# Kernel optimization log

Hardware: AMD Instinct MI355X
Metric: run time of the kernel (lower is better)

The kernel has to match this reference:

```python
import jax, jax.numpy as jnp
import numpy as np

B, N, M = 2, 4096, 4096
QUERY_DIM, CONTEXT_DIM = 512, 768
H, D = 8, 64
INNER = H * D


def setup_inputs() -> dict:
    key = jax.random.key(0)
    ks = jax.random.split(key, 8)
    x = jax.random.normal(ks[0], (B, N, QUERY_DIM), dtype=jnp.float32)
    context_tensor = jax.random.normal(ks[1], (B, M, CONTEXT_DIM), dtype=jnp.float32)
    mask = jax.random.randint(ks[2], (B, M), 0, 2) > 0  # bool [B, M]
    s = 0.02
    Wq = jax.random.normal(ks[3], (QUERY_DIM, INNER), dtype=jnp.float32) * s
    Wk = jax.random.normal(ks[4], (CONTEXT_DIM, INNER), dtype=jnp.float32) * s
    Wv = jax.random.normal(ks[5], (CONTEXT_DIM, INNER), dtype=jnp.float32) * s
    Wo = jax.random.normal(ks[6], (INNER, QUERY_DIM), dtype=jnp.float32) * s
    bo = jnp.zeros((QUERY_DIM,), dtype=jnp.float32)
    return {"x": x, "context_tensor": context_tensor, "mask": mask,
            "Wq": Wq, "Wk": Wk, "Wv": Wv, "Wo": Wo, "bo": bo}


def reference(x, context_tensor, mask, Wq, Wk, Wv, Wo, bo):
    scale = D ** (-0.5)
    # projections -> [B, T, H, D]
    q = (x @ Wq).reshape(B, N, H, D)
    k = (context_tensor @ Wk).reshape(B, M, H, D)
    v = (context_tensor @ Wv).reshape(B, M, H, D)
    # scores [B, H, N, M]
    attn = jnp.einsum('bnhd,bmhd->bhnm', q, k) * scale
    neg = -jnp.finfo(attn.dtype).max
    attn = jnp.where(mask[:, None, None, :], attn, neg)
    attn = jax.nn.softmax(attn, axis=-1)
    out = jnp.einsum('bhnm,bmhd->bnhd', attn, v).reshape(B, N, INNER)
    return out @ Wo + bo  # dropout is 0.0 -> identity
```

## Files before the change

kernel.cpp:

```cpp
#include <hip/hip_runtime.h>

typedef unsigned short u16;
typedef unsigned int u32;
typedef __attribute__((ext_vector_type(8))) short bf16x8;
typedef __attribute__((ext_vector_type(4))) short bf16x4;
typedef __attribute__((ext_vector_type(4))) float f32x4;

#define CSC 0.1803368801111244f

__device__ __forceinline__ u16 f2b(float f) {
  union { float f; u32 u; } c; c.f = f;
  return (u16)((c.u + 0x8000u) >> 16);
}

__device__ __forceinline__ uint2 pk4(f32x4 p) {
  union { float f; u32 u; } c0, c1, c2, c3;
  c0.f = p[0]; c1.f = p[1]; c2.f = p[2]; c3.f = p[3];
  u32 a = c0.u + 0x8000u, b = c1.u + 0x8000u;
  u32 c = c2.u + 0x8000u, d = c3.u + 0x8000u;
  uint2 r;
  r.x = __builtin_amdgcn_perm(b, a, 0x07060302u);
  r.y = __builtin_amdgcn_perm(d, c, 0x07060302u);
  return r;
}

__device__ __forceinline__ bf16x4 pk4v(f32x4 p) {
  union { uint2 u; bf16x4 v; } c;
  c.u = pk4(p);
  return c.v;
}

__device__ __forceinline__ void async16(const void* g, void* s) {
  __builtin_amdgcn_global_load_lds(
      (const __attribute__((address_space(1))) u32*)g,
      (__attribute__((address_space(3))) u32*)s, 16, 0, 0);
}

__global__ void prep(const float* __restrict__ x, const float* __restrict__ ctx,
                     const int* __restrict__ mask,
                     const float* __restrict__ Wq, const float* __restrict__ Wk,
                     const float* __restrict__ Wv, const float* __restrict__ Wo,
                     u16* __restrict__ Xb, u16* __restrict__ Cb,
                     float* __restrict__ mvalid, float* __restrict__ cnt,
                     u16* __restrict__ Wtq, u16* __restrict__ Wtkv, u16* __restrict__ Wto) {
  __shared__ u16 Tl[64 * 65];
  __shared__ int cred[4];
  const int bid = blockIdx.x, tid = threadIdx.x;
  if (bid < 10240) {
    const float* src; u16* dst; int i;
    if (bid < 4096) { i = (bid * 256 + tid) * 4; src = x; dst = Xb; }
    else { i = ((bid - 4096) * 256 + tid) * 4; src = ctx; dst = Cb; }
    float4 f = *(const float4*)&src[i];
    ushort4 o;
    o.x = f2b(f.x); o.y = f2b(f.y); o.z = f2b(f.z); o.w = f2b(f.w);
    *(ushort4*)&dst[i] = o;
  } else if (bid < 10560) {
    int t = bid - 10240;
    const float* W; u16* Wt; int Kd, tt;
    if (t < 64)       { W = Wq; Wt = Wtq;  Kd = 512; tt = t; }
    else if (t < 160) { W = Wk; Wt = Wtkv; Kd = 768; tt = t - 64; }
    else if (t < 256) { W = Wv; Wt = Wtkv + (size_t)512 * 768; Kd = 768; tt = t - 160; }
    else              { W = Wo; Wt = Wto;  Kd = 512; tt = t - 256; }
    const int k0 = (tt >> 3) * 64, n0 = (tt & 7) * 64;
    {
      const int r = tid >> 2, cg = (tid & 3) * 16;
#pragma unroll
      for (int i = 0; i < 4; i++) {
        float4 f = *(const float4*)&W[(size_t)(k0 + r) * 512 + n0 + cg + i * 4];
        Tl[r * 65 + cg + i * 4 + 0] = f2b(f.x);
        Tl[r * 65 + cg + i * 4 + 1] = f2b(f.y);
        Tl[r * 65 + cg + i * 4 + 2] = f2b(f.z);
        Tl[r * 65 + cg + i * 4 + 3] = f2b(f.w);
      }
    }
    __syncthreads();
    {
      const int n = tid >> 2, kg = (tid & 3) * 16;
      u16 buf[16];
#pragma unroll
      for (int i = 0; i < 16; i++) buf[i] = Tl[(kg + i) * 65 + n];
      u16* dst = &Wt[(size_t)(n0 + n) * Kd + k0 + kg];
      *(uint4*)dst = *(const uint4*)&buf[0];
      *(uint4*)(dst + 8) = *(const uint4*)&buf[8];
    }
  } else {
    const int b = bid - 10560;
    const int base = b * 4096;
    const int w = tid >> 6, lane = tid & 63;
    int zc = 0;
#pragma unroll
    for (int j = 0; j < 16; j++) {
      int idx = tid + j * 256;
      int mv = mask[base + idx];
      mvalid[base + idx] = mv ? 1.f : 0.f;
      zc += (mv == 0);
    }
#pragma unroll
    for (int d = 1; d < 64; d <<= 1) zc += __shfl_xor(zc, d);
    if (lane == 0) cred[w] = zc;
    __syncthreads();
    if (tid == 0) cnt[b] = (float)(cred[0] + cred[1] + cred[2] + cred[3]);
  }
}

__global__ __launch_bounds__(256, 6)
void gemm_qkv(const u16* __restrict__ Xb, const u16* __restrict__ Cb,
              const u16* __restrict__ Wtq, const u16* __restrict__ Wtkv,
              const float* __restrict__ mvalid,
              u16* __restrict__ Qb, u16* __restrict__ Kb, u16* __restrict__ Vt) {
  __shared__ u16 As[64 * 64];
  __shared__ u16 Bs[128 * 64];
  const int tid = threadIdx.x;
  const int w = tid >> 6, lane = tid & 63, quad = lane >> 4, l16 = lane & 15;
  const int wr = w >> 1, wc = w & 1;
  const int y = blockIdx.y;
  const bool isQ = (y < 4);
  const u16* A  = isQ ? Xb : Cb;
  const u16* Bt = isQ ? Wtq : Wtkv;
  const int K   = isQ ? 512 : 768;
  const int n0  = isQ ? y * 128 : (y - 4) * 128;
  const size_t m0 = (size_t)blockIdx.x * 64;
  const u16* Ab = A + m0 * K;
  const u16* Bb = Bt + (size_t)n0 * K;

  const int cswz = (((lane & 7) ^ ((lane >> 3) & 7)) << 3);
  const int sw0 = ((quad ^ (l16 & 7)) << 3);
  const int sw1 = sw0 ^ 32;
  const int r8 = lane >> 3;

  f32x4 acc[2][4];
#pragma unroll
  for (int i = 0; i < 2; i++)
#pragma unroll
    for (int j = 0; j < 4; j++) acc[i][j] = (f32x4){0.f, 0.f, 0.f, 0.f};

  for (int k0 = 0; k0 < K; k0 += 64) {
    async16(Ab + (size_t)(w * 16 + r8) * K + k0 + cswz, &As[(w * 16) * 64]);
    async16(Ab + (size_t)(w * 16 + 8 + r8) * K + k0 + cswz, &As[(w * 16 + 8) * 64]);
#pragma unroll
    for (int t = 0; t < 4; t++)
      async16(Bb + (size_t)(w * 32 + t * 8 + r8) * K + k0 + cswz, &Bs[(w * 32 + t * 8) * 64]);
    __syncthreads();
#pragma unroll
    for (int ks = 0; ks < 2; ks++) {
      const int so = ks ? sw1 : sw0;
      bf16x8 af[2], bfr[4];
#pragma unroll
      for (int i = 0; i < 2; i++)
        af[i] = *(const bf16x8*)&As[(wr * 32 + i * 16 + l16) * 64 + so];
#pragma unroll
      for (int j = 0; j < 4; j++)
        bfr[j] = *(const bf16x8*)&Bs[(wc * 64 + j * 16 + l16) * 64 + so];
#pragma unroll
      for (int i = 0; i < 2; i++)
#pragma unroll
        for (int j = 0; j < 4; j++)
          acc[i][j] = __builtin_amdgcn_mfma_f32_16x16x32_bf16(af[i], bfr[j], acc[i][j], 0, 0, 0);
    }
    __syncthreads();
  }

  if (isQ) {
#pragma unroll
    for (int i = 0; i < 2; i++)
#pragma unroll
      for (int j = 0; j < 4; j++)
#pragma unroll
        for (int r = 0; r < 4; r++) {
          size_t row = m0 + wr * 32 + i * 16 + quad * 4 + r;
          Qb[row * 512 + n0 + wc * 64 + j * 16 + l16] = f2b(acc[i][j][r]);
        }
  } else if (n0 < 512) {
#pragma unroll
    for (int i = 0; i < 2; i++) {
      size_t row0 = m0 + wr * 32 + i * 16 + quad * 4;
      f32x4 vm = *(const f32x4*)&mvalid[row0];
#pragma unroll
      for (int j = 0; j < 4; j++)
#pragma unroll
        for (int r = 0; r < 4; r++)
          Kb[(row0 + r) * 512 + n0 + wc * 64 + j * 16 + l16] = f2b(acc[i][j][r] * (vm[r] * CSC));
    }
  } else {
#pragma unroll
    for (int i = 0; i < 2; i++) {
      size_t row0 = m0 + wr * 32 + i * 16 + quad * 4;
      f32x4 vm = *(const f32x4*)&mvalid[row0];
#pragma unroll
      for (int j = 0; j < 4; j++) {
        int d = n0 - 512 + wc * 64 + j * 16 + l16;
        f32x4 v;
#pragma unroll
        for (int r = 0; r < 4; r++) v[r] = acc[i][j][r] * vm[r];
        *(uint2*)&Vt[(size_t)d * 8192 + row0] = pk4(v);
      }
    }
  }
}

__global__ __launch_bounds__(256, 4)
void gemm_o(const u16* __restrict__ A, const u16* __restrict__ Bt,
            const float* __restrict__ bias, float* __restrict__ Cf) {
  __shared__ u16 As[64 * 64];
  __shared__ u16 Bs[64 * 64];
  const int tid = threadIdx.x;
  const int w = tid >> 6, lane = tid & 63, quad = lane >> 4, l16 = lane & 15;
  const size_t m0 = (size_t)blockIdx.x * 64;
  const int n0 = blockIdx.y * 64;
  const u16* Ab = A + m0 * 512;
  const u16* Bb = Bt + (size_t)n0 * 512;

  const int cswz = (((lane & 7) ^ ((lane >> 3) & 7)) << 3);
  const int sw0 = ((quad ^ (l16 & 7)) << 3);
  const int sw1 = sw0 ^ 32;
  const int r8 = lane >> 3;

  f32x4 acc[4];
#pragma unroll
  for (int j = 0; j < 4; j++) acc[j] = (f32x4){0.f, 0.f, 0.f, 0.f};

  for (int k0 = 0; k0 < 512; k0 += 64) {
    async16(Ab + (size_t)(w * 16 + r8) * 512 + k0 + cswz, &As[(w * 16) * 64]);
    async16(Ab + (size_t)(w * 16 + 8 + r8) * 512 + k0 + cswz, &As[(w * 16 + 8) * 64]);
    async16(Bb + (size_t)(w * 16 + r8) * 512 + k0 + cswz, &Bs[(w * 16) * 64]);
    async16(Bb + (size_t)(w * 16 + 8 + r8) * 512 + k0 + cswz, &Bs[(w * 16 + 8) * 64]);
    __syncthreads();
#pragma unroll
    for (int ks = 0; ks < 2; ks++) {
      const int so = ks ? sw1 : sw0;
      bf16x8 af = *(const bf16x8*)&As[(w * 16 + l16) * 64 + so];
#pragma unroll
      for (int j = 0; j < 4; j++) {
        bf16x8 bfr = *(const bf16x8*)&Bs[(j * 16 + l16) * 64 + so];
        acc[j] = __builtin_amdgcn_mfma_f32_16x16x32_bf16(af, bfr, acc[j], 0, 0, 0);
      }
    }
    __syncthreads();
  }

#pragma unroll
  for (int j = 0; j < 4; j++)
#pragma unroll
    for (int r = 0; r < 4; r++) {
      size_t row = m0 + w * 16 + quad * 4 + r;
      int col = n0 + j * 16 + l16;
      Cf[row * 512 + col] = acc[j][r] + bias[col];
    }
}

__global__ __launch_bounds__(256, 4)
void attn_kernel(const u16* __restrict__ Q, const u16* __restrict__ Kg,
                 const u16* __restrict__ Vt, const float* __restrict__ cnt,
                 u16* __restrict__ AO) {
  __shared__ u16 Ks[2][64 * 64];
  __shared__ u16 Vs[2][64 * 64];

  const int tid = threadIdx.x;
  const int w = tid >> 6, lane = tid & 63, quad = lane >> 4, l16 = lane & 15;
  const int l = blockIdx.x;
  const int qb = l >> 4, hb = l & 15, h = hb >> 1, b = hb & 1;
  const size_t qrow0 = (size_t)b * 4096 + (size_t)qb * 64;
  const size_t crow0 = (size_t)b * 4096;
  const int hcol = h * 64;
  const float cb = cnt[b];

  const int cswz = (((lane & 7) ^ ((lane >> 3) & 7)) << 3);
  const int sw0 = ((quad ^ (l16 & 7)) << 3);
  const int sw1 = sw0 ^ 32;
  const int r8 = lane >> 3;

  bf16x8 qf[2];
#pragma unroll
  for (int ks = 0; ks < 2; ks++)
    qf[ks] = *(const bf16x8*)&Q[(qrow0 + w * 16 + l16) * 512 + hcol + ks * 32 + quad * 8];

  async16(Kg + (crow0 + w * 16 + r8) * 512 + hcol + cswz, &Ks[0][(w * 16) * 64]);
  async16(Kg + (crow0 + w * 16 + 8 + r8) * 512 + hcol + cswz, &Ks[0][(w * 16 + 8) * 64]);
  async16(Vt + (size_t)(hcol + w * 16 + r8) * 8192 + crow0 + cswz, &Vs[0][(w * 16) * 64]);
  async16(Vt + (size_t)(hcol + w * 16 + 8 + r8) * 8192 + crow0 + cswz, &Vs[0][(w * 16 + 8) * 64]);
  __syncthreads();

  f32x4 Oacc[4];
#pragma unroll
  for (int dt = 0; dt < 4; dt++) Oacc[dt] = (f32x4){0.f, 0.f, 0.f, 0.f};
  float lsum = 0.f;

  for (int mt = 0; mt < 64; mt++) {
    const int cur = mt & 1;
    const size_t m0 = (size_t)mt * 64;

    if (mt < 63) {
      const size_t mn = m0 + 64;
      async16(Kg + (crow0 + mn + w * 16 + r8) * 512 + hcol + cswz, &Ks[cur ^ 1][(w * 16) * 64]);
      async16(Kg + (crow0 + mn + w * 16 + 8 + r8) * 512 + hcol + cswz, &Ks[cur ^ 1][(w * 16 + 8) * 64]);
      async16(Vt + (size_t)(hcol + w * 16 + r8) * 8192 + crow0 + mn + cswz, &Vs[cur ^ 1][(w * 16) * 64]);
      async16(Vt + (size_t)(hcol + w * 16 + 8 + r8) * 8192 + crow0 + mn + cswz, &Vs[cur ^ 1][(w * 16 + 8) * 64]);
    }

    f32x4 sacc[4];
#pragma unroll
    for (int mtt = 0; mtt < 4; mtt++) sacc[mtt] = (f32x4){0.f, 0.f, 0.f, 0.f};
#pragma unroll
    for (int ks = 0; ks < 2; ks++) {
      const int so = ks ? sw1 : sw0;
#pragma unroll
      for (int mtt = 0; mtt < 4; mtt++) {
        bf16x8 kb = *(const bf16x8*)&Ks[cur][(mtt * 16 + l16) * 64 + so];
        sacc[mtt] = __builtin_amdgcn_mfma_f32_16x16x32_bf16(kb, qf[ks], sacc[mtt], 0, 0, 0);
      }
    }

    bf16x4 pf[4];
#pragma unroll
    for (int mtt = 0; mtt < 4; mtt++) {
      f32x4 p;
#pragma unroll
      for (int r = 0; r < 4; r++) {
        p[r] = __builtin_amdgcn_exp2f(sacc[mtt][r]);
        lsum += p[r];
      }
      pf[mtt] = pk4v(p);
    }

#pragma unroll
    for (int mtt = 0; mtt < 4; mtt++) {
#pragma unroll
      for (int dt = 0; dt < 4; dt++) {
        bf16x4 va = *(const bf16x4*)&Vs[cur][(dt * 16 + l16) * 64 +
                      (((mtt * 2 + (quad >> 1)) ^ (l16 & 7)) << 3) + ((quad & 1) << 2)];
        Oacc[dt] = __builtin_amdgcn_mfma_f32_16x16x16bf16_1k(va, pf[mtt], Oacc[dt], 0, 0, 0);
      }
    }
    __syncthreads();
  }

  lsum += __shfl_xor(lsum, 16);
  lsum += __shfl_xor(lsum, 32);
  const float inv = 1.0f / (lsum - cb);

#pragma unroll
  for (int dt = 0; dt < 4; dt++) {
    f32x4 o;
#pragma unroll
    for (int r = 0; r < 4; r++) o[r] = Oacc[dt][r] * inv;
    *(uint2*)&AO[(qrow0 + w * 16 + l16) * 512 + hcol + dt * 16 + quad * 4] = pk4(o);
  }
}


extern "C" void kernel_launch(void* const* d_in, const int* in_sizes, int n_in,
                              void* d_out, int out_size, void* d_ws, size_t ws_size,
                              hipStream_t stream) {
  const float* x   = (const float*)d_in[0];
  const float* ctx = (const float*)d_in[1];
  const int*  mask = (const int*)d_in[2];
  const float* Wq  = (const float*)d_in[3];
  const float* Wk  = (const float*)d_in[4];
  const float* Wv  = (const float*)d_in[5];
  const float* Wo  = (const float*)d_in[6];
  const float* bo  = (const float*)d_in[7];
  float* out = (float*)d_out;

  char* p = (char*)d_ws;
  u16* Xb   = (u16*)p; p += (size_t)8192 * 512 * 2;
  u16* Cb   = (u16*)p; p += (size_t)8192 * 768 * 2;
  u16* Wtq  = (u16*)p; p += (size_t)512 * 512 * 2;
  u16* Wtkv = (u16*)p; p += (size_t)1024 * 768 * 2;
  u16* Wto  = (u16*)p; p += (size_t)512 * 512 * 2;
  u16* Qb   = (u16*)p; p += (size_t)8192 * 512 * 2;
  u16* Kb   = (u16*)p; p += (size_t)8192 * 512 * 2;
  u16* Vtg  = (u16*)p; p += (size_t)512 * 8192 * 2;
  u16* AOb  = (u16*)p; p += (size_t)8192 * 512 * 2;
  float* mvalid = (float*)p; p += (size_t)8192 * 4;
  float* cnt    = (float*)p; p += 2 * 4;

  prep<<<10562, 256, 0, stream>>>(x, ctx, mask, Wq, Wk, Wv, Wo,
                                  Xb, Cb, mvalid, cnt, Wtq, Wtkv, Wto);
  gemm_qkv<<<dim3(128, 12), 256, 0, stream>>>(Xb, Cb, Wtq, Wtkv, mvalid, Qb, Kb, Vtg);
  attn_kernel<<<1024, 256, 0, stream>>>(Qb, Kb, Vtg, cnt, AOb);
  gemm_o<<<dim3(128, 8), 256, 0, stream>>>(AOb, Wto, bo, out);
}
```

Baseline: 229.8 us.

## Split attention warps 2x2 over query and key tiles with LDS reduction

Each warp previously owned 16 query rows and walked all 64 keys of a tile. Now the four warps form a 2x2 grid: each handles 32 query rows against a 32-key half. K and V fragments loaded from LDS are each reused across two query subtiles, roughly halving LDS reads per MFMA. Partial outputs and row sums from the two key halves are combined through shared memory at the end, and the bf16 pack for P switches to the hardware v_cvt_pk_bf16_f32 instruction. The cost is more accumulator registers per warp (two Oacc sets) and an extra reduction step with a barrier.

```diff
diff --git a/kernel.cpp b/kernel.cpp
--- a/kernel.cpp
+++ b/kernel.cpp
@@ -24,9 +24,10 @@
   return r;
 }
 
-__device__ __forceinline__ bf16x4 pk4v(f32x4 p) {
+__device__ __forceinline__ bf16x4 pk4cvt(f32x4 p) {
   union { uint2 u; bf16x4 v; } c;
-  c.u = pk4(p);
+  asm("v_cvt_pk_bf16_f32 %0, %1, %2" : "=v"(c.u.x) : "v"(p[0]), "v"(p[1]));
+  asm("v_cvt_pk_bf16_f32 %0, %1, %2" : "=v"(c.u.y) : "v"(p[2]), "v"(p[3]));
   return c.v;
 }
 
@@ -257,6 +258,7 @@
 
   const int tid = threadIdx.x;
   const int w = tid >> 6, lane = tid & 63, quad = lane >> 4, l16 = lane & 15;
+  const int wq = w >> 1, wm = w & 1;
   const int l = blockIdx.x;
   const int qb = l >> 4, hb = l & 15, h = hb >> 1, b = hb & 1;
   const size_t qrow0 = (size_t)b * 4096 + (size_t)qb * 64;
@@ -269,10 +271,13 @@
   const int sw1 = sw0 ^ 32;
   const int r8 = lane >> 3;
 
-  bf16x8 qf[2];
-#pragma unroll
-  for (int ks = 0; ks < 2; ks++)
-    qf[ks] = *(const bf16x8*)&Q[(qrow0 + w * 16 + l16) * 512 + hcol + ks * 32 + quad * 8];
+  bf16x8 qf[2][2];
+#pragma unroll
+  for (int qt = 0; qt < 2; qt++)
+#pragma unroll
+    for (int ks = 0; ks < 2; ks++)
+      qf[qt][ks] = *(const bf16x8*)&Q[(qrow0 + wq * 32 + qt * 16 + l16) * 512 +
+                                      hcol + ks * 32 + quad * 8];
 
   async16(Kg + (crow0 + w * 16 + r8) * 512 + hcol + cswz, &Ks[0][(w * 16) * 64]);
   async16(Kg + (crow0 + w * 16 + 8 + r8) * 512 + hcol + cswz, &Ks[0][(w * 16 + 8) * 64]);
@@ -280,10 +285,12 @@
   async16(Vt + (size_t)(hcol + w * 16 + 8 + r8) * 8192 + crow0 + cswz, &Vs[0][(w * 16 + 8) * 64]);
   __syncthreads();
 
-  f32x4 Oacc[4];
-#pragma unroll
-  for (int dt = 0; dt < 4; dt++) Oacc[dt] = (f32x4){0.f, 0.f, 0.f, 0.f};
-  float lsum = 0.f;
+  f32x4 Oacc[2][4];
+#pragma unroll
+  for (int qt = 0; qt < 2; qt++)
+#pragma unroll
+    for (int dt = 0; dt < 4; dt++) Oacc[qt][dt] = (f32x4){0.f, 0.f, 0.f, 0.f};
+  float lsum[2] = {0.f, 0.f};
 
   for (int mt = 0; mt < 64; mt++) {
     const int cur = mt & 1;
@@ -297,53 +304,82 @@
       async16(Vt + (size_t)(hcol + w * 16 + 8 + r8) * 8192 + crow0 + mn + cswz, &Vs[cur ^ 1][(w * 16 + 8) * 64]);
     }
 
-    f32x4 sacc[4];
-#pragma unroll
-    for (int mtt = 0; mtt < 4; mtt++) sacc[mtt] = (f32x4){0.f, 0.f, 0.f, 0.f};
+    f32x4 sacc[2][2];
+#pragma unroll
+    for (int qt = 0; qt < 2; qt++)
+#pragma unroll
+      for (int mtt = 0; mtt < 2; mtt++) sacc[qt][mtt] = (f32x4){0.f, 0.f, 0.f, 0.f};
 #pragma unroll
     for (int ks = 0; ks < 2; ks++) {
       const int so = ks ? sw1 : sw0;
 #pragma unroll
-      for (int mtt = 0; mtt < 4; mtt++) {
-        bf16x8 kb = *(const bf16x8*)&Ks[cur][(mtt * 16 + l16) * 64 + so];
-        sacc[mtt] = __builtin_amdgcn_mfma_f32_16x16x32_bf16(kb, qf[ks], sacc[mtt], 0, 0, 0);
-      }
-    }
-
-    bf16x4 pf[4];
-#pragma unroll
-    for (int mtt = 0; mtt < 4; mtt++) {
-      f32x4 p;
-#pragma unroll
-      for (int r = 0; r < 4; r++) {
-        p[r] = __builtin_amdgcn_exp2f(sacc[mtt][r]);
-        lsum += p[r];
-      }
-      pf[mtt] = pk4v(p);
-    }
-
-#pragma unroll
-    for (int mtt = 0; mtt < 4; mtt++) {
+      for (int mtt = 0; mtt < 2; mtt++) {
+        bf16x8 kb = *(const bf16x8*)&Ks[cur][(wm * 32 + mtt * 16 + l16) * 64 + so];
+#pragma unroll
+        for (int qt = 0; qt < 2; qt++)
+          sacc[qt][mtt] = __builtin_amdgcn_mfma_f32_16x16x32_bf16(kb, qf[qt][ks], sacc[qt][mtt], 0, 0, 0);
+      }
+    }
+
+    bf16x4 pf[2][2];
+#pragma unroll
+    for (int qt = 0; qt < 2; qt++)
+#pragma unroll
+      for (int mtt = 0; mtt < 2; mtt++) {
+        f32x4 p;
+#pragma unroll
+        for (int r = 0; r < 4; r++) {
+          p[r] = __builtin_amdgcn_exp2f(sacc[qt][mtt][r]);
+          lsum[qt] += p[r];
+        }
+        pf[qt][mtt] = pk4cvt(p);
+      }
+
+#pragma unroll
+    for (int mtt = 0; mtt < 2; mtt++) {
 #pragma unroll
       for (int dt = 0; dt < 4; dt++) {
         bf16x4 va = *(const bf16x4*)&Vs[cur][(dt * 16 + l16) * 64 +
-                      (((mtt * 2 + (quad >> 1)) ^ (l16 & 7)) << 3) + ((quad & 1) << 2)];
-        Oacc[dt] = __builtin_amdgcn_mfma_f32_16x16x16bf16_1k(va, pf[mtt], Oacc[dt], 0, 0, 0);
-      }
-    }
-    __syncthreads();
-  }
-
-  lsum += __shfl_xor(lsum, 16);
-  lsum += __shfl_xor(lsum, 32);
-  const float inv = 1.0f / (lsum - cb);
-
-#pragma unroll
-  for (int dt = 0; dt < 4; dt++) {
-    f32x4 o;
-#pragma unroll
-    for (int r = 0; r < 4; r++) o[r] = Oacc[dt][r] * inv;
-    *(uint2*)&AO[(qrow0 + w * 16 + l16) * 512 + hcol + dt * 16 + quad * 4] = pk4(o);
+                      (((wm * 4 + mtt * 2 + (quad >> 1)) ^ (l16 & 7)) << 3) + ((quad & 1) << 2)];
+#pragma unroll
+        for (int qt = 0; qt < 2; qt++)
+          Oacc[qt][dt] = __builtin_amdgcn_mfma_f32_16x16x16bf16_1k(va, pf[qt][mtt], Oacc[qt][dt], 0, 0, 0);
+      }
+    }
+    __syncthreads();
+  }
+
+#pragma unroll
+  for (int qt = 0; qt < 2; qt++) {
+    lsum[qt] += __shfl_xor(lsum[qt], 16);
+    lsum[qt] += __shfl_xor(lsum[qt], 32);
+  }
+
+  float* red  = (float*)&Ks[0][0];
+  float* lred = (float*)&Vs[0][0];
+  if (wm == 1) {
+#pragma unroll
+    for (int qt = 0; qt < 2; qt++) {
+#pragma unroll
+      for (int dt = 0; dt < 4; dt++)
+        *(f32x4*)&red[wq * 2048 + (qt * 4 + dt) * 256 + lane * 4] = Oacc[qt][dt];
+      lred[wq * 128 + qt * 64 + lane] = lsum[qt];
+    }
+  }
+  __syncthreads();
+  if (wm == 0) {
+#pragma unroll
+    for (int qt = 0; qt < 2; qt++) {
+      const float inv = 1.0f / (lsum[qt] + lred[wq * 128 + qt * 64 + lane] - cb);
+#pragma unroll
+      for (int dt = 0; dt < 4; dt++) {
+        f32x4 part = *(const f32x4*)&red[wq * 2048 + (qt * 4 + dt) * 256 + lane * 4];
+        f32x4 o;
+#pragma unroll
+        for (int r = 0; r < 4; r++) o[r] = (Oacc[qt][dt][r] + part[r]) * inv;
+        *(uint2*)&AO[(qrow0 + wq * 32 + qt * 16 + l16) * 512 + hcol + dt * 16 + quad * 4] = pk4(o);
+      }
+    }
   }
 }
 
```

Result: faster. 215.1 us, median of 2 (-6.4%).
